# Optimization experiments

Hardware: AMD Instinct MI355X
Metric: run time of the kernel (lower is better)

The kernel has to match this reference:

```python
import jax, jax.numpy as jnp
from jax import lax
import numpy as np

SEQ, BATCH, IN, HID = 512, 256, 248, 1024


def setup_inputs() -> dict:
    key = jax.random.key(0)
    ks = jax.random.split(key, 9)
    s_in = 1.0 / np.sqrt(HID)  # pytorch default init scale for RNN/Linear
    x = jax.random.normal(ks[0], (SEQ, BATCH, IN), dtype=jnp.float32)
    W_ih = jax.random.uniform(ks[1], (HID, IN), jnp.float32, -s_in, s_in)
    b_ih = jax.random.uniform(ks[2], (HID,), jnp.float32, -s_in, s_in)
    W_hh = jax.random.uniform(ks[3], (HID, HID), jnp.float32, -s_in, s_in)
    b_hh = jax.random.uniform(ks[4], (HID,), jnp.float32, -s_in, s_in)
    W_out = jax.random.uniform(ks[5], (1, HID), jnp.float32, -s_in, s_in)
    b_out = jax.random.uniform(ks[6], (1,), jnp.float32, -s_in, s_in)
    w_r = jax.random.uniform(ks[7], (1, 1), jnp.float32, -1.0, 1.0)
    b_r = jax.random.uniform(ks[8], (1,), jnp.float32, -1.0, 1.0)
    return {"x": x, "W_ih": W_ih, "b_ih": b_ih, "W_hh": W_hh, "b_hh": b_hh,
            "W_out": W_out, "b_out": b_out, "w_r": w_r, "b_r": b_r}


def reference(x, W_ih, b_ih, W_hh, b_hh, W_out, b_out, w_r, b_r):
    # x: (T, B, IN) time-major, like torch nn.RNN default.
    T, B, _ = x.shape
    H = W_hh.shape[0]
    # Precompute input projection for all timesteps: (T, B, H)
    xproj = jnp.einsum('tbi,hi->tbh', x, W_ih) + b_ih + b_hh

    def rnn_step(h, xp):
        h_new = jnp.tanh(xp + h @ W_hh.T)
        return h_new, h_new

    h0 = jnp.zeros((B, H), dtype=x.dtype)
    _, hs = lax.scan(rnn_step, h0, xproj)  # hs: (T, B, H)

    # Output logits for all timesteps: (T, B, 1)
    z = jnp.einsum('tbh,oh->tbo', hs, W_out) + b_out

    # o_0 = sigmoid(z_0); o_t = sigmoid(z_t + recurr(o_{t-1}))
    o0 = jax.nn.sigmoid(z[0])

    def out_step(o_prev, zt):
        o = jax.nn.sigmoid(zt + o_prev @ w_r.T + b_r)
        return o, o

    _, os = lax.scan(out_step, o0, z[1:])
    o_all = jnp.concatenate([o0[None], os], axis=0)  # (T, B, 1)
    return o_all[:, :, 0].T  # (B, T), matching oFinal
```

## Files before the change

### kernel.cpp

```cpp
#include <hip/hip_runtime.h>

#define T_SEQ 512
#define NB    256
#define NIN   248
#define NH    1024

typedef __attribute__((ext_vector_type(8))) short          short8;
typedef __attribute__((ext_vector_type(4))) float          f32x4;
typedef __attribute__((ext_vector_type(4))) unsigned int   uint4v;
typedef __attribute__((ext_vector_type(4))) float          float4v;
typedef unsigned long long u64;

#define AS_RELAXED __ATOMIC_RELAXED
#define AS_AGENT   __HIP_MEMORY_SCOPE_AGENT

__device__ __forceinline__ unsigned short f2bf(float f){
  unsigned int u = __float_as_uint(f);
  u += 0x7FFFu + ((u >> 16) & 1u);
  return (unsigned short)(u >> 16);
}

__device__ __forceinline__ float tanh_fast(float v){
  float e = __expf(2.0f * v);
  return 1.0f - 2.0f / (e + 1.0f);
}

__launch_bounds__(256, 1)
__global__ void rnn_scan_kernel(const float* __restrict__ x,
                                const float* __restrict__ W_ih,
                                const float* __restrict__ b_ih,
                                const float* __restrict__ W_hh,
                                const float* __restrict__ b_hh,
                                const float* __restrict__ W_out,
                                unsigned short* __restrict__ hbuf,
                                float* __restrict__ z,
                                unsigned int* __restrict__ bar)
{
  __shared__ alignas(16) unsigned short h_frag[2048 * 8];
  __shared__ alignas(16) unsigned short x_frag[512 * 8];
  __shared__ alignas(8)  unsigned short h_out[16 * 64];
  __shared__ float z_hist[T_SEQ * 16];

  const int tid    = threadIdx.x;
  const int wg     = blockIdx.x;
  const int r16    = wg & 15;
  const int bg     = (r16 & 7) * 2 + (r16 >> 3);
  const int jg     = wg >> 4;
  const int b_base = bg * 16;
  const int l      = tid & 63;
  const int wv     = tid >> 6;
  const int n      = l & 15;
  const int quad   = l >> 4;
  const int j      = jg * 64 + wv * 16 + n;

  unsigned short* h0 = hbuf;
  unsigned short* h1 = hbuf + (size_t)NB * NH;
  unsigned int* ctr  = bar + bg * 32;

  short8 whh[32];
  #pragma unroll
  for (int kt = 0; kt < 32; ++kt){
    const float* p = W_hh + (size_t)j * NH + kt * 32 + quad * 8;
    float4v a = *(const float4v*)p;
    float4v b = *(const float4v*)(p + 4);
    short8 v;
    v[0]=(short)f2bf(a[0]); v[1]=(short)f2bf(a[1]); v[2]=(short)f2bf(a[2]); v[3]=(short)f2bf(a[3]);
    v[4]=(short)f2bf(b[0]); v[5]=(short)f2bf(b[1]); v[6]=(short)f2bf(b[2]); v[7]=(short)f2bf(b[3]);
    whh[kt] = v;
  }
  short8 wih[8];
  #pragma unroll
  for (int kt = 0; kt < 8; ++kt){
    short8 v = {0,0,0,0,0,0,0,0};
    if (!(kt == 7 && quad == 3)){
      const float* p = W_ih + (size_t)j * NIN + kt * 32 + quad * 8;
      float4v a = *(const float4v*)p;
      float4v b = *(const float4v*)(p + 4);
      v[0]=(short)f2bf(a[0]); v[1]=(short)f2bf(a[1]); v[2]=(short)f2bf(a[2]); v[3]=(short)f2bf(a[3]);
      v[4]=(short)f2bf(b[0]); v[5]=(short)f2bf(b[1]); v[6]=(short)f2bf(b[2]); v[7]=(short)f2bf(b[3]);
    }
    wih[kt] = v;
  }
  const float bias  = b_ih[j] + b_hh[j];
  const float woutj = W_out[j];

  #pragma unroll
  for (int i = 0; i < 32; ++i) z_hist[tid + i * 256] = 0.f;
  {
    int r = tid >> 4, c = (tid & 15) * 4;
    __hip_atomic_store((u64*)&h0[(size_t)(b_base + r) * NH + jg * 64 + c],
                       0ull, AS_RELAXED, AS_AGENT);
    int tt = jg * 32 + (tid >> 3);
    int bb = (tid & 7) * 2;
    __hip_atomic_store(&z[(size_t)tt * NB + b_base + bb],     0.f, AS_RELAXED, AS_AGENT);
    __hip_atomic_store(&z[(size_t)tt * NB + b_base + bb + 1], 0.f, AS_RELAXED, AS_AGENT);
  }

  const int xslot_kt[2] = { tid >> 6, (tid + 256) >> 6 };
  const int xslot_l2[2] = { tid & 63, tid & 63 };
  float4v xr[2][2];
  bool    xvalid[2];
  #pragma unroll
  for (int i = 0; i < 2; ++i){
    int kt = xslot_kt[i], l2 = xslot_l2[i];
    int b = b_base + (l2 & 15), k = kt * 32 + (l2 >> 4) * 8;
    xvalid[i] = !(kt == 7 && (l2 >> 4) == 3);
    if (xvalid[i]){
      const float* p = x + ((size_t)0 * NB + b) * NIN + k;
      xr[i][0] = *(const float4v*)p;
      xr[i][1] = *(const float4v*)(p + 4);
    }
  }

  unsigned int target = 16;
  __syncthreads();
  if (tid == 0){
    __hip_atomic_fetch_add(ctr, 1u, AS_RELAXED, AS_AGENT);
    while (__hip_atomic_load(ctr, AS_RELAXED, AS_AGENT) < target)
      __builtin_amdgcn_s_sleep(1);
  }
  __syncthreads();

  for (int t = 0; t < T_SEQ; ++t){
    const unsigned short* hp = (t & 1) ? h1 : h0;
    unsigned short*       hn = (t & 1) ? h0 : h1;

    #pragma unroll
    for (int i = 0; i < 8; ++i){
      int slot = tid + i * 256;
      int kt = slot >> 6, l2 = slot & 63;
      int b = b_base + (l2 & 15), k = kt * 32 + (l2 >> 4) * 8;
      const u64* src = (const u64*)(hp + (size_t)b * NH + k);
      u64 w0 = __hip_atomic_load(src,     AS_RELAXED, AS_AGENT);
      u64 w1 = __hip_atomic_load(src + 1, AS_RELAXED, AS_AGENT);
      u64* dst = (u64*)&h_frag[slot * 8];
      dst[0] = w0; dst[1] = w1;
    }
    #pragma unroll
    for (int i = 0; i < 2; ++i){
      int slot = tid + i * 256;
      uint4v v = {0u,0u,0u,0u};
      if (xvalid[i]){
        v[0] = (unsigned)f2bf(xr[i][0][0]) | ((unsigned)f2bf(xr[i][0][1]) << 16);
        v[1] = (unsigned)f2bf(xr[i][0][2]) | ((unsigned)f2bf(xr[i][0][3]) << 16);
        v[2] = (unsigned)f2bf(xr[i][1][0]) | ((unsigned)f2bf(xr[i][1][1]) << 16);
        v[3] = (unsigned)f2bf(xr[i][1][2]) | ((unsigned)f2bf(xr[i][1][3]) << 16);
      }
      *(uint4v*)&x_frag[slot * 8] = v;
    }
    __syncthreads();

    f32x4 acc0 = {bias, bias, bias, bias};
    f32x4 acc1 = {0.f, 0.f, 0.f, 0.f};
    #pragma unroll
    for (int kt = 0; kt < 32; kt += 2){
      short8 a0 = *(const short8*)&h_frag[(kt * 64 + l) * 8];
      short8 a1 = *(const short8*)&h_frag[((kt + 1) * 64 + l) * 8];
      acc0 = __builtin_amdgcn_mfma_f32_16x16x32_bf16(a0, whh[kt],     acc0, 0, 0, 0);
      acc1 = __builtin_amdgcn_mfma_f32_16x16x32_bf16(a1, whh[kt + 1], acc1, 0, 0, 0);
    }
    #pragma unroll
    for (int kt = 0; kt < 8; kt += 2){
      short8 a0 = *(const short8*)&x_frag[(kt * 64 + l) * 8];
      short8 a1 = *(const short8*)&x_frag[((kt + 1) * 64 + l) * 8];
      acc0 = __builtin_amdgcn_mfma_f32_16x16x32_bf16(a0, wih[kt],     acc0, 0, 0, 0);
      acc1 = __builtin_amdgcn_mfma_f32_16x16x32_bf16(a1, wih[kt + 1], acc1, 0, 0, 0);
    }

    {
      int tn = (t + 1 < T_SEQ) ? t + 1 : t;
      #pragma unroll
      for (int i = 0; i < 2; ++i){
        if (xvalid[i]){
          int kt = xslot_kt[i], l2 = xslot_l2[i];
          int b = b_base + (l2 & 15), k = kt * 32 + (l2 >> 4) * 8;
          const float* p = x + ((size_t)tn * NB + b) * NIN + k;
          xr[i][0] = *(const float4v*)p;
          xr[i][1] = *(const float4v*)(p + 4);
        }
      }
    }

    float hv[4];
    #pragma unroll
    for (int i = 0; i < 4; ++i){
      hv[i] = tanh_fast(acc0[i] + acc1[i]);
      h_out[(quad * 4 + i) * 64 + wv * 16 + n] = f2bf(hv[i]);
    }
    float sv[4];
    #pragma unroll
    for (int i = 0; i < 4; ++i) sv[i] = hv[i] * woutj;
    #pragma unroll
    for (int m = 1; m < 16; m <<= 1){
      #pragma unroll
      for (int i = 0; i < 4; ++i) sv[i] += __shfl_xor(sv[i], m, 64);
    }
    if (n == 0){
      #pragma unroll
      for (int i = 0; i < 4; ++i) atomicAdd(&z_hist[t * 16 + quad * 4 + i], sv[i]);
    }
    __syncthreads();

    {
      int r = tid >> 4, c = (tid & 15) * 4;
      u64 v = *(const u64*)&h_out[r * 64 + c];
      __hip_atomic_store((u64*)&hn[(size_t)(b_base + r) * NH + jg * 64 + c],
                         v, AS_RELAXED, AS_AGENT);
    }

    target += 16;
    __syncthreads();
    if (tid == 0){
      __hip_atomic_fetch_add(ctr, 1u, AS_RELAXED, AS_AGENT);
      while (__hip_atomic_load(ctr, AS_RELAXED, AS_AGENT) < target)
        __builtin_amdgcn_s_sleep(1);
    }
    __syncthreads();
  }

  __syncthreads();
  #pragma unroll
  for (int i = 0; i < 32; ++i){
    int idx = tid + i * 256;
    int tt = idx >> 4, bb = idx & 15;
    atomicAdd(&z[(size_t)tt * NB + b_base + bb], z_hist[idx]);
  }
}

__global__ void out_scan_kernel(const float* __restrict__ z,
                                const float* __restrict__ b_out,
                                const float* __restrict__ w_r,
                                const float* __restrict__ b_r,
                                float* __restrict__ out)
{
  int b = threadIdx.x;
  float bo = b_out[0], wr = w_r[0], br = b_r[0];
  float o = 0.f;
  for (int t = 0; t < T_SEQ; ++t){
    float pre = z[(size_t)t * NB + b] + bo;
    if (t > 0) pre += wr * o + br;
    o = 1.0f / (1.0f + __expf(-pre));
    out[(size_t)b * T_SEQ + t] = o;
  }
}

extern "C" void kernel_launch(void* const* d_in, const int* in_sizes, int n_in,
                              void* d_out, int out_size, void* d_ws, size_t ws_size,
                              hipStream_t stream)
{
  (void)in_sizes; (void)n_in; (void)out_size; (void)ws_size;
  const float* x     = (const float*)d_in[0];
  const float* W_ih  = (const float*)d_in[1];
  const float* b_ih  = (const float*)d_in[2];
  const float* W_hh  = (const float*)d_in[3];
  const float* b_hh  = (const float*)d_in[4];
  const float* W_out = (const float*)d_in[5];
  const float* b_out = (const float*)d_in[6];
  const float* w_r   = (const float*)d_in[7];
  const float* b_r   = (const float*)d_in[8];
  float* out = (float*)d_out;

  unsigned short* hbuf = (unsigned short*)d_ws;
  float* z = (float*)((char*)d_ws + 2 * (size_t)NB * NH * sizeof(unsigned short));
  unsigned int* bar = (unsigned int*)((char*)d_ws
                        + 2 * (size_t)NB * NH * sizeof(unsigned short)
                        + (size_t)T_SEQ * NB * sizeof(float));

  hipMemsetAsync(bar, 0, 16 * 32 * sizeof(unsigned int), stream);

  rnn_scan_kernel<<<dim3(256), dim3(256), 0, stream>>>(
      x, W_ih, b_ih, W_hh, b_hh, W_out, hbuf, z, bar);

  out_scan_kernel<<<dim3(1), dim3(256), 0, stream>>>(z, b_out, w_r, b_r, out);
}
```

Baseline: 2.699 ms.

## Replace counter barrier with per-workgroup step flags and split MFMA accumulators

Replaces the shared fetch-add counter barrier across the 16 workgroups of a batch group with per-workgroup monotonic flags. Each workgroup publishes its step with a store, and every wave polls the 16 flags before loading h, so the atomic RMW contention and the extra block-wide syncs go away. It also batches the global h loads into registers before writing LDS, splits the MFMA chain into four accumulators for more ILP, and moves the W_out reduction after the h store so it overlaps with publication. In exchange it relies on relaxed-ordering visibility of the h stores before the flag store with no explicit fence, and it raises register pressure.

```diff
diff --git a/kernel.cpp b/kernel.cpp
--- a/kernel.cpp
+++ b/kernel.cpp
@@ -55,7 +55,7 @@
 
   unsigned short* h0 = hbuf;
   unsigned short* h1 = hbuf + (size_t)NB * NH;
-  unsigned int* ctr  = bar + bg * 32;
+  unsigned int* flags = bar + bg * 32;
 
   short8 whh[32];
   #pragma unroll
@@ -112,29 +112,30 @@
     }
   }
 
-  unsigned int target = 16;
   __syncthreads();
-  if (tid == 0){
-    __hip_atomic_fetch_add(ctr, 1u, AS_RELAXED, AS_AGENT);
-    while (__hip_atomic_load(ctr, AS_RELAXED, AS_AGENT) < target)
-      __builtin_amdgcn_s_sleep(1);
-  }
-  __syncthreads();
+  if (tid == 0)
+    __hip_atomic_store(&flags[jg], 1u, AS_RELAXED, AS_AGENT);
 
   for (int t = 0; t < T_SEQ; ++t){
     const unsigned short* hp = (t & 1) ? h1 : h0;
     unsigned short*       hn = (t & 1) ? h0 : h1;
 
+    {
+      const unsigned int tgt = (unsigned)(t + 1);
+      const unsigned int* f = &flags[l & 15];
+      while (__hip_atomic_load(f, AS_RELAXED, AS_AGENT) < tgt)
+        __builtin_amdgcn_s_sleep(1);
+    }
+
+    u64 hw0[8], hw1[8];
     #pragma unroll
     for (int i = 0; i < 8; ++i){
       int slot = tid + i * 256;
       int kt = slot >> 6, l2 = slot & 63;
       int b = b_base + (l2 & 15), k = kt * 32 + (l2 >> 4) * 8;
       const u64* src = (const u64*)(hp + (size_t)b * NH + k);
-      u64 w0 = __hip_atomic_load(src,     AS_RELAXED, AS_AGENT);
-      u64 w1 = __hip_atomic_load(src + 1, AS_RELAXED, AS_AGENT);
-      u64* dst = (u64*)&h_frag[slot * 8];
-      dst[0] = w0; dst[1] = w1;
+      hw0[i] = __hip_atomic_load(src,     AS_RELAXED, AS_AGENT);
+      hw1[i] = __hip_atomic_load(src + 1, AS_RELAXED, AS_AGENT);
     }
     #pragma unroll
     for (int i = 0; i < 2; ++i){
@@ -148,23 +149,38 @@
       }
       *(uint4v*)&x_frag[slot * 8] = v;
     }
+    #pragma unroll
+    for (int i = 0; i < 8; ++i){
+      u64* dst = (u64*)&h_frag[(tid + i * 256) * 8];
+      dst[0] = hw0[i]; dst[1] = hw1[i];
+    }
     __syncthreads();
 
-    f32x4 acc0 = {bias, bias, bias, bias};
-    f32x4 acc1 = {0.f, 0.f, 0.f, 0.f};
-    #pragma unroll
-    for (int kt = 0; kt < 32; kt += 2){
-      short8 a0 = *(const short8*)&h_frag[(kt * 64 + l) * 8];
-      short8 a1 = *(const short8*)&h_frag[((kt + 1) * 64 + l) * 8];
-      acc0 = __builtin_amdgcn_mfma_f32_16x16x32_bf16(a0, whh[kt],     acc0, 0, 0, 0);
-      acc1 = __builtin_amdgcn_mfma_f32_16x16x32_bf16(a1, whh[kt + 1], acc1, 0, 0, 0);
-    }
-    #pragma unroll
-    for (int kt = 0; kt < 8; kt += 2){
-      short8 a0 = *(const short8*)&x_frag[(kt * 64 + l) * 8];
-      short8 a1 = *(const short8*)&x_frag[((kt + 1) * 64 + l) * 8];
-      acc0 = __builtin_amdgcn_mfma_f32_16x16x32_bf16(a0, wih[kt],     acc0, 0, 0, 0);
-      acc1 = __builtin_amdgcn_mfma_f32_16x16x32_bf16(a1, wih[kt + 1], acc1, 0, 0, 0);
+    f32x4 a0 = {bias, bias, bias, bias};
+    f32x4 a1 = {0.f, 0.f, 0.f, 0.f};
+    f32x4 a2 = {0.f, 0.f, 0.f, 0.f};
+    f32x4 a3 = {0.f, 0.f, 0.f, 0.f};
+    #pragma unroll
+    for (int kt = 0; kt < 32; kt += 4){
+      short8 f0 = *(const short8*)&h_frag[((kt + 0) * 64 + l) * 8];
+      short8 f1 = *(const short8*)&h_frag[((kt + 1) * 64 + l) * 8];
+      short8 f2 = *(const short8*)&h_frag[((kt + 2) * 64 + l) * 8];
+      short8 f3 = *(const short8*)&h_frag[((kt + 3) * 64 + l) * 8];
+      a0 = __builtin_amdgcn_mfma_f32_16x16x32_bf16(f0, whh[kt + 0], a0, 0, 0, 0);
+      a1 = __builtin_amdgcn_mfma_f32_16x16x32_bf16(f1, whh[kt + 1], a1, 0, 0, 0);
+      a2 = __builtin_amdgcn_mfma_f32_16x16x32_bf16(f2, whh[kt + 2], a2, 0, 0, 0);
+      a3 = __builtin_amdgcn_mfma_f32_16x16x32_bf16(f3, whh[kt + 3], a3, 0, 0, 0);
+    }
+    #pragma unroll
+    for (int kt = 0; kt < 8; kt += 4){
+      short8 f0 = *(const short8*)&x_frag[((kt + 0) * 64 + l) * 8];
+      short8 f1 = *(const short8*)&x_frag[((kt + 1) * 64 + l) * 8];
+      short8 f2 = *(const short8*)&x_frag[((kt + 2) * 64 + l) * 8];
+      short8 f3 = *(const short8*)&x_frag[((kt + 3) * 64 + l) * 8];
+      a0 = __builtin_amdgcn_mfma_f32_16x16x32_bf16(f0, wih[kt + 0], a0, 0, 0, 0);
+      a1 = __builtin_amdgcn_mfma_f32_16x16x32_bf16(f1, wih[kt + 1], a1, 0, 0, 0);
+      a2 = __builtin_amdgcn_mfma_f32_16x16x32_bf16(f2, wih[kt + 2], a2, 0, 0, 0);
+      a3 = __builtin_amdgcn_mfma_f32_16x16x32_bf16(f3, wih[kt + 3], a3, 0, 0, 0);
     }
 
     {
@@ -184,20 +200,8 @@
     float hv[4];
     #pragma unroll
     for (int i = 0; i < 4; ++i){
-      hv[i] = tanh_fast(acc0[i] + acc1[i]);
+      hv[i] = tanh_fast(a0[i] + a1[i] + a2[i] + a3[i]);
       h_out[(quad * 4 + i) * 64 + wv * 16 + n] = f2bf(hv[i]);
-    }
-    float sv[4];
-    #pragma unroll
-    for (int i = 0; i < 4; ++i) sv[i] = hv[i] * woutj;
-    #pragma unroll
-    for (int m = 1; m < 16; m <<= 1){
-      #pragma unroll
-      for (int i = 0; i < 4; ++i) sv[i] += __shfl_xor(sv[i], m, 64);
-    }
-    if (n == 0){
-      #pragma unroll
-      for (int i = 0; i < 4; ++i) atomicAdd(&z_hist[t * 16 + quad * 4 + i], sv[i]);
     }
     __syncthreads();
 
@@ -207,15 +211,22 @@
       __hip_atomic_store((u64*)&hn[(size_t)(b_base + r) * NH + jg * 64 + c],
                          v, AS_RELAXED, AS_AGENT);
     }
-
-    target += 16;
+    float sv[4];
+    #pragma unroll
+    for (int i = 0; i < 4; ++i) sv[i] = hv[i] * woutj;
+    #pragma unroll
+    for (int m = 1; m < 16; m <<= 1){
+      #pragma unroll
+      for (int i = 0; i < 4; ++i) sv[i] += __shfl_xor(sv[i], m, 64);
+    }
+    if (n == 0){
+      #pragma unroll
+      for (int i = 0; i < 4; ++i) atomicAdd(&z_hist[t * 16 + quad * 4 + i], sv[i]);
+    }
+
     __syncthreads();
-    if (tid == 0){
-      __hip_atomic_fetch_add(ctr, 1u, AS_RELAXED, AS_AGENT);
-      while (__hip_atomic_load(ctr, AS_RELAXED, AS_AGENT) < target)
-        __builtin_amdgcn_s_sleep(1);
-    }
-    __syncthreads();
+    if (tid == 0)
+      __hip_atomic_store(&flags[jg], (unsigned)(t + 2), AS_RELAXED, AS_AGENT);
   }
 
   __syncthreads();
```

After: 2.250 ms. 1.2x faster.

## Ping-pong two batch groups per workgroup with per-wave flag barriers

Applied to the files above, without the earlier changes.

Each workgroup now handles two 16-row batch groups (A and B) and alternates between them, so the global h load for one group overlaps the MFMA and tanh work of the other. This hides the latency of the cross-workgroup synchronization. The single counter barrier with s_sleep is replaced by per-wave monotonic flags that every lane polls, which also removes the trailing __syncthreads. The grid is halved to 128 workgroups, which doubles LDS and register use per workgroup. Ordering now rests on relaxed atomics plus vmcnt waits, which carries a memory-ordering risk.

```diff
diff --git a/kernel.cpp b/kernel.cpp
--- a/kernel.cpp
+++ b/kernel.cpp
@@ -19,10 +19,28 @@
   u += 0x7FFFu + ((u >> 16) & 1u);
   return (unsigned short)(u >> 16);
 }
-
+__device__ __forceinline__ unsigned pk2(float lo, float hi){
+  return (unsigned)f2bf(lo) | ((unsigned)f2bf(hi) << 16);
+}
 __device__ __forceinline__ float tanh_fast(float v){
   float e = __expf(2.0f * v);
   return 1.0f - 2.0f / (e + 1.0f);
+}
+
+__device__ __forceinline__ void barrier_lds(){
+  asm volatile("s_waitcnt lgkmcnt(0)" ::: "memory");
+  __builtin_amdgcn_s_barrier();
+  __builtin_amdgcn_sched_barrier(0);
+}
+
+__device__ __forceinline__ void wait_flags(unsigned spec, const unsigned* fl,
+                                           int l, unsigned tgt){
+  if (__all((int)(spec >= tgt))) return;
+  unsigned v;
+  do {
+    __builtin_amdgcn_s_sleep(1);
+    v = __hip_atomic_load(&fl[l], AS_RELAXED, AS_AGENT);
+  } while (!__all((int)(v >= tgt)));
 }
 
 __launch_bounds__(256, 1)
@@ -36,17 +54,20 @@
                                 float* __restrict__ z,
                                 unsigned int* __restrict__ bar)
 {
-  __shared__ alignas(16) unsigned short h_frag[2048 * 8];
-  __shared__ alignas(16) unsigned short x_frag[512 * 8];
-  __shared__ alignas(8)  unsigned short h_out[16 * 64];
-  __shared__ float z_hist[T_SEQ * 16];
+  __shared__ alignas(16) unsigned short h_fragA[2048 * 8];
+  __shared__ alignas(16) unsigned short h_fragB[2048 * 8];
+  __shared__ alignas(16) unsigned short x_fragA[512 * 8];
+  __shared__ alignas(16) unsigned short x_fragB[512 * 8];
+  __shared__ alignas(8)  unsigned short h_out[4 * 256];
+  __shared__ float z_histA[T_SEQ * 16];
+  __shared__ float z_histB[T_SEQ * 16];
 
   const int tid    = threadIdx.x;
   const int wg     = blockIdx.x;
-  const int r16    = wg & 15;
-  const int bg     = (r16 & 7) * 2 + (r16 >> 3);
-  const int jg     = wg >> 4;
-  const int b_base = bg * 16;
+  const int pairId = wg & 7;
+  const int jg     = wg >> 3;
+  const int b_baseA = pairId * 32;
+  const int b_baseB = pairId * 32 + 16;
   const int l      = tid & 63;
   const int wv     = tid >> 6;
   const int n      = l & 15;
@@ -55,7 +76,8 @@
 
   unsigned short* h0 = hbuf;
   unsigned short* h1 = hbuf + (size_t)NB * NH;
-  unsigned int* ctr  = bar + bg * 32;
+  unsigned int* flagsA = bar + pairId * 128;
+  unsigned int* flagsB = bar + pairId * 128 + 64;
 
   short8 whh[32];
   #pragma unroll
@@ -85,137 +107,175 @@
   const float woutj = W_out[j];
 
   #pragma unroll
-  for (int i = 0; i < 32; ++i) z_hist[tid + i * 256] = 0.f;
+  for (int i = 0; i < 32; ++i){
+    z_histA[tid + i * 256] = 0.f;
+    z_histB[tid + i * 256] = 0.f;
+  }
   {
-    int r = tid >> 4, c = (tid & 15) * 4;
-    __hip_atomic_store((u64*)&h0[(size_t)(b_base + r) * NH + jg * 64 + c],
-                       0ull, AS_RELAXED, AS_AGENT);
+    int r = l >> 2, c = (l & 3) * 4;
+    size_t col = (size_t)jg * 64 + wv * 16 + c;
+    __hip_atomic_store((u64*)&h0[(size_t)(b_baseA + r) * NH + col], 0ull, AS_RELAXED, AS_AGENT);
+    __hip_atomic_store((u64*)&h0[(size_t)(b_baseB + r) * NH + col], 0ull, AS_RELAXED, AS_AGENT);
     int tt = jg * 32 + (tid >> 3);
     int bb = (tid & 7) * 2;
-    __hip_atomic_store(&z[(size_t)tt * NB + b_base + bb],     0.f, AS_RELAXED, AS_AGENT);
-    __hip_atomic_store(&z[(size_t)tt * NB + b_base + bb + 1], 0.f, AS_RELAXED, AS_AGENT);
+    __hip_atomic_store(&z[(size_t)tt * NB + b_baseA + bb],     0.f, AS_RELAXED, AS_AGENT);
+    __hip_atomic_store(&z[(size_t)tt * NB + b_baseA + bb + 1], 0.f, AS_RELAXED, AS_AGENT);
+    __hip_atomic_store(&z[(size_t)tt * NB + b_baseB + bb],     0.f, AS_RELAXED, AS_AGENT);
+    __hip_atomic_store(&z[(size_t)tt * NB + b_baseB + bb + 1], 0.f, AS_RELAXED, AS_AGENT);
+  }
+  asm volatile("s_waitcnt vmcnt(0)" ::: "memory");
+  if (l == 0){
+    __hip_atomic_store(&flagsA[jg * 4 + wv], 1u, AS_RELAXED, AS_AGENT);
+    __hip_atomic_store(&flagsB[jg * 4 + wv], 1u, AS_RELAXED, AS_AGENT);
   }
 
   const int xslot_kt[2] = { tid >> 6, (tid + 256) >> 6 };
   const int xslot_l2[2] = { tid & 63, tid & 63 };
-  float4v xr[2][2];
-  bool    xvalid[2];
-  #pragma unroll
-  for (int i = 0; i < 2; ++i){
-    int kt = xslot_kt[i], l2 = xslot_l2[i];
-    int b = b_base + (l2 & 15), k = kt * 32 + (l2 >> 4) * 8;
-    xvalid[i] = !(kt == 7 && (l2 >> 4) == 3);
-    if (xvalid[i]){
-      const float* p = x + ((size_t)0 * NB + b) * NIN + k;
-      xr[i][0] = *(const float4v*)p;
-      xr[i][1] = *(const float4v*)(p + 4);
-    }
-  }
-
-  unsigned int target = 16;
-  __syncthreads();
-  if (tid == 0){
-    __hip_atomic_fetch_add(ctr, 1u, AS_RELAXED, AS_AGENT);
-    while (__hip_atomic_load(ctr, AS_RELAXED, AS_AGENT) < target)
-      __builtin_amdgcn_s_sleep(1);
-  }
-  __syncthreads();
+  bool xvalid[2];
+  #pragma unroll
+  for (int i = 0; i < 2; ++i)
+    xvalid[i] = !(xslot_kt[i] == 7 && (xslot_l2[i] >> 4) == 3);
+
+  float4v xrA[2][2], xrB[2][2];
+  u64 hwA0[8], hwA1[8], hwB0[8], hwB1[8];
+  unsigned fA = 0, fB = 0;
+
+#define XPREF(XR, BBASE, TN)                                               \
+  _Pragma("unroll")                                                        \
+  for (int i = 0; i < 2; ++i){                                             \
+    if (xvalid[i]){                                                        \
+      int kt = xslot_kt[i], l2 = xslot_l2[i];                              \
+      int b = (BBASE) + (l2 & 15), k = kt * 32 + (l2 >> 4) * 8;            \
+      const float* p = x + ((size_t)(TN) * NB + b) * NIN + k;              \
+      XR[i][0] = *(const float4v*)p;                                       \
+      XR[i][1] = *(const float4v*)(p + 4);                                 \
+    }                                                                      \
+  }
+
+#define STAGE_H(HF, HW0, HW1)                                              \
+  _Pragma("unroll")                                                        \
+  for (int i = 0; i < 8; ++i){                                             \
+    u64* dst = (u64*)&HF[(tid + i * 256) * 8];                             \
+    dst[0] = HW0[i]; dst[1] = HW1[i];                                      \
+  }
+
+#define STAGE_X(XF, XR)                                                    \
+  _Pragma("unroll")                                                        \
+  for (int i = 0; i < 2; ++i){                                             \
+    uint4v v = {0u,0u,0u,0u};                                              \
+    if (xvalid[i]){                                                        \
+      v[0] = pk2(XR[i][0][0], XR[i][0][1]);                                \
+      v[1] = pk2(XR[i][0][2], XR[i][0][3]);                                \
+      v[2] = pk2(XR[i][1][0], XR[i][1][1]);                                \
+      v[3] = pk2(XR[i][1][2], XR[i][1][3]);                                \
+    }                                                                      \
+    *(uint4v*)&XF[(tid + i * 256) * 8] = v;                                \
+  }
+
+#define LOAD_H(HW0, HW1, HSRC, BBASE)                                      \
+  _Pragma("unroll")                                                        \
+  for (int i = 0; i < 8; ++i){                                             \
+    int slot = tid + i * 256;                                              \
+    int kt = slot >> 6, l2 = slot & 63;                                    \
+    const u64* src = (const u64*)((HSRC)                                   \
+        + (size_t)((BBASE) + (l2 & 15)) * NH + kt * 32 + (l2 >> 4) * 8);   \
+    HW0[i] = __hip_atomic_load(src,     AS_RELAXED, AS_AGENT);             \
+    HW1[i] = __hip_atomic_load(src + 1, AS_RELAXED, AS_AGENT);             \
+  }
+
+#define MFMA_TILE(HF, XF, A0, A1, A2, A3)                                  \
+  _Pragma("unroll")                                                        \
+  for (int kt = 0; kt < 32; kt += 4){                                      \
+    short8 q0 = *(const short8*)&HF[((kt + 0) * 64 + l) * 8];              \
+    short8 q1 = *(const short8*)&HF[((kt + 1) * 64 + l) * 8];              \
+    short8 q2 = *(const short8*)&HF[((kt + 2) * 64 + l) * 8];              \
+    short8 q3 = *(const short8*)&HF[((kt + 3) * 64 + l) * 8];              \
+    A0 = __builtin_amdgcn_mfma_f32_16x16x32_bf16(q0, whh[kt + 0], A0, 0, 0, 0); \
+    A1 = __builtin_amdgcn_mfma_f32_16x16x32_bf16(q1, whh[kt + 1], A1, 0, 0, 0); \
+    A2 = __builtin_amdgcn_mfma_f32_16x16x32_bf16(q2, whh[kt + 2], A2, 0, 0, 0); \
+    A3 = __builtin_amdgcn_mfma_f32_16x16x32_bf16(q3, whh[kt + 3], A3, 0, 0, 0); \
+  }                                                                        \
+  _Pragma("unroll")                                                        \
+  for (int kt = 0; kt < 8; kt += 4){                                       \
+    short8 q0 = *(const short8*)&XF[((kt + 0) * 64 + l) * 8];              \
+    short8 q1 = *(const short8*)&XF[((kt + 1) * 64 + l) * 8];              \
+    short8 q2 = *(const short8*)&XF[((kt + 2) * 64 + l) * 8];              \
+    short8 q3 = *(const short8*)&XF[((kt + 3) * 64 + l) * 8];              \
+    A0 = __builtin_amdgcn_mfma_f32_16x16x32_bf16(q0, wih[kt + 0], A0, 0, 0, 0); \
+    A1 = __builtin_amdgcn_mfma_f32_16x16x32_bf16(q1, wih[kt + 1], A1, 0, 0, 0); \
+    A2 = __builtin_amdgcn_mfma_f32_16x16x32_bf16(q2, wih[kt + 2], A2, 0, 0, 0); \
+    A3 = __builtin_amdgcn_mfma_f32_16x16x32_bf16(q3, wih[kt + 3], A3, 0, 0, 0); \
+  }
+
+#define FINISH(A0, A1, A2, A3, ZH, BBASE, FLAGS, TPUB)                     \
+  {                                                                        \
+    float sv[4];                                                           \
+    _Pragma("unroll")                                                      \
+    for (int i = 0; i < 4; ++i){                                           \
+      float hvv = tanh_fast(A0[i] + A1[i] + A2[i] + A3[i]);                \
+      h_out[wv * 256 + (quad * 4 + i) * 16 + n] = f2bf(hvv);               \
+      sv[i] = hvv * woutj;                                                 \
+    }                                                                      \
+    _Pragma("unroll")                                                      \
+    for (int m = 1; m < 16; m <<= 1){                                      \
+      _Pragma("unroll")                                                    \
+      for (int i = 0; i < 4; ++i) sv[i] += __shfl_xor(sv[i], m, 64);       \
+    }                                                                      \
+    if (n == 0){                                                           \
+      _Pragma("unroll")                                                    \
+      for (int i = 0; i < 4; ++i)                                          \
+        atomicAdd(&ZH[t * 16 + quad * 4 + i], sv[i]);                      \
+    }                                                                      \
+    {                                                                      \
+      int r = l >> 2, c = (l & 3) * 4;                                     \
+      u64 v = *(const u64*)&h_out[wv * 256 + r * 16 + c];                  \
+      __hip_atomic_store((u64*)&hn[(size_t)((BBASE) + r) * NH              \
+                         + jg * 64 + wv * 16 + c], v, AS_RELAXED, AS_AGENT); \
+    }                                                                      \
+    asm volatile("s_waitcnt vmcnt(0)" ::: "memory");                       \
+    if (l == 0)                                                            \
+      __hip_atomic_store(&FLAGS[jg * 4 + wv], (unsigned)(TPUB),            \
+                         AS_RELAXED, AS_AGENT);                            \
+  }
+
+  wait_flags(0u, flagsA, l, 1u);
+  LOAD_H(hwA0, hwA1, h0, b_baseA);
+  fB = __hip_atomic_load(&flagsB[l], AS_RELAXED, AS_AGENT);
+  XPREF(xrA, b_baseA, 0);
+  XPREF(xrB, b_baseB, 0);
 
   for (int t = 0; t < T_SEQ; ++t){
     const unsigned short* hp = (t & 1) ? h1 : h0;
     unsigned short*       hn = (t & 1) ? h0 : h1;
-
-    #pragma unroll
-    for (int i = 0; i < 8; ++i){
-      int slot = tid + i * 256;
-      int kt = slot >> 6, l2 = slot & 63;
-      int b = b_base + (l2 & 15), k = kt * 32 + (l2 >> 4) * 8;
-      const u64* src = (const u64*)(hp + (size_t)b * NH + k);
-      u64 w0 = __hip_atomic_load(src,     AS_RELAXED, AS_AGENT);
-      u64 w1 = __hip_atomic_load(src + 1, AS_RELAXED, AS_AGENT);
-      u64* dst = (u64*)&h_frag[slot * 8];
-      dst[0] = w0; dst[1] = w1;
-    }
-    #pragma unroll
-    for (int i = 0; i < 2; ++i){
-      int slot = tid + i * 256;
-      uint4v v = {0u,0u,0u,0u};
-      if (xvalid[i]){
-        v[0] = (unsigned)f2bf(xr[i][0][0]) | ((unsigned)f2bf(xr[i][0][1]) << 16);
-        v[1] = (unsigned)f2bf(xr[i][0][2]) | ((unsigned)f2bf(xr[i][0][3]) << 16);
-        v[2] = (unsigned)f2bf(xr[i][1][0]) | ((unsigned)f2bf(xr[i][1][1]) << 16);
-        v[3] = (unsigned)f2bf(xr[i][1][2]) | ((unsigned)f2bf(xr[i][1][3]) << 16);
-      }
-      *(uint4v*)&x_frag[slot * 8] = v;
-    }
-    __syncthreads();
-
-    f32x4 acc0 = {bias, bias, bias, bias};
-    f32x4 acc1 = {0.f, 0.f, 0.f, 0.f};
-    #pragma unroll
-    for (int kt = 0; kt < 32; kt += 2){
-      short8 a0 = *(const short8*)&h_frag[(kt * 64 + l) * 8];
-      short8 a1 = *(const short8*)&h_frag[((kt + 1) * 64 + l) * 8];
-      acc0 = __builtin_amdgcn_mfma_f32_16x16x32_bf16(a0, whh[kt],     acc0, 0, 0, 0);
-      acc1 = __builtin_amdgcn_mfma_f32_16x16x32_bf16(a1, whh[kt + 1], acc1, 0, 0, 0);
-    }
-    #pragma unroll
-    for (int kt = 0; kt < 8; kt += 2){
-      short8 a0 = *(const short8*)&x_frag[(kt * 64 + l) * 8];
-      short8 a1 = *(const short8*)&x_frag[((kt + 1) * 64 + l) * 8];
-      acc0 = __builtin_amdgcn_mfma_f32_16x16x32_bf16(a0, wih[kt],     acc0, 0, 0, 0);
-      acc1 = __builtin_amdgcn_mfma_f32_16x16x32_bf16(a1, wih[kt + 1], acc1, 0, 0, 0);
-    }
-
-    {
-      int tn = (t + 1 < T_SEQ) ? t + 1 : t;
-      #pragma unroll
-      for (int i = 0; i < 2; ++i){
-        if (xvalid[i]){
-          int kt = xslot_kt[i], l2 = xslot_l2[i];
-          int b = b_base + (l2 & 15), k = kt * 32 + (l2 >> 4) * 8;
-          const float* p = x + ((size_t)tn * NB + b) * NIN + k;
-          xr[i][0] = *(const float4v*)p;
-          xr[i][1] = *(const float4v*)(p + 4);
-        }
-      }
-    }
-
-    float hv[4];
-    #pragma unroll
-    for (int i = 0; i < 4; ++i){
-      hv[i] = tanh_fast(acc0[i] + acc1[i]);
-      h_out[(quad * 4 + i) * 64 + wv * 16 + n] = f2bf(hv[i]);
-    }
-    float sv[4];
-    #pragma unroll
-    for (int i = 0; i < 4; ++i) sv[i] = hv[i] * woutj;
-    #pragma unroll
-    for (int m = 1; m < 16; m <<= 1){
-      #pragma unroll
-      for (int i = 0; i < 4; ++i) sv[i] += __shfl_xor(sv[i], m, 64);
-    }
-    if (n == 0){
-      #pragma unroll
-      for (int i = 0; i < 4; ++i) atomicAdd(&z_hist[t * 16 + quad * 4 + i], sv[i]);
-    }
-    __syncthreads();
-
-    {
-      int r = tid >> 4, c = (tid & 15) * 4;
-      u64 v = *(const u64*)&h_out[r * 64 + c];
-      __hip_atomic_store((u64*)&hn[(size_t)(b_base + r) * NH + jg * 64 + c],
-                         v, AS_RELAXED, AS_AGENT);
-    }
-
-    target += 16;
-    __syncthreads();
-    if (tid == 0){
-      __hip_atomic_fetch_add(ctr, 1u, AS_RELAXED, AS_AGENT);
-      while (__hip_atomic_load(ctr, AS_RELAXED, AS_AGENT) < target)
-        __builtin_amdgcn_s_sleep(1);
-    }
-    __syncthreads();
+    const int tn = (t + 1 < T_SEQ) ? t + 1 : t;
+
+    STAGE_H(h_fragA, hwA0, hwA1);
+    wait_flags(fB, flagsB, l, (unsigned)(t + 1));
+    LOAD_H(hwB0, hwB1, hp, b_baseB);
+    STAGE_X(x_fragA, xrA);
+    XPREF(xrA, b_baseA, tn);
+    barrier_lds();
+    f32x4 a0 = {bias, bias, bias, bias};
+    f32x4 a1 = {0.f, 0.f, 0.f, 0.f};
+    f32x4 a2 = {0.f, 0.f, 0.f, 0.f};
+    f32x4 a3 = {0.f, 0.f, 0.f, 0.f};
+    MFMA_TILE(h_fragA, x_fragA, a0, a1, a2, a3);
+    FINISH(a0, a1, a2, a3, z_histA, b_baseA, flagsA, t + 2);
+    fA = __hip_atomic_load(&flagsA[l], AS_RELAXED, AS_AGENT);
+
+    STAGE_H(h_fragB, hwB0, hwB1);
+    wait_flags(fA, flagsA, l, (unsigned)(t + 2));
+    LOAD_H(hwA0, hwA1, hn, b_baseA);
+    STAGE_X(x_fragB, xrB);
+    XPREF(xrB, b_baseB, tn);
+    barrier_lds();
+    f32x4 b0 = {bias, bias, bias, bias};
+    f32x4 b1 = {0.f, 0.f, 0.f, 0.f};
+    f32x4 b2 = {0.f, 0.f, 0.f, 0.f};
+    f32x4 b3 = {0.f, 0.f, 0.f, 0.f};
+    MFMA_TILE(h_fragB, x_fragB, b0, b1, b2, b3);
+    FINISH(b0, b1, b2, b3, z_histB, b_baseB, flagsB, t + 2);
+    fB = __hip_atomic_load(&flagsB[l], AS_RELAXED, AS_AGENT);
   }
 
   __syncthreads();
@@ -223,8 +283,16 @@
   for (int i = 0; i < 32; ++i){
     int idx = tid + i * 256;
     int tt = idx >> 4, bb = idx & 15;
-    atomicAdd(&z[(size_t)tt * NB + b_base + bb], z_hist[idx]);
-  }
+    atomicAdd(&z[(size_t)tt * NB + b_baseA + bb], z_histA[idx]);
+    atomicAdd(&z[(size_t)tt * NB + b_baseB + bb], z_histB[idx]);
+  }
+
+#undef XPREF
+#undef STAGE_H
+#undef STAGE_X
+#undef LOAD_H
+#undef MFMA_TILE
+#undef FINISH
 }
 
 __global__ void out_scan_kernel(const float* __restrict__ z,
@@ -266,9 +334,9 @@
                         + 2 * (size_t)NB * NH * sizeof(unsigned short)
                         + (size_t)T_SEQ * NB * sizeof(float));
 
-  hipMemsetAsync(bar, 0, 16 * 32 * sizeof(unsigned int), stream);
-
-  rnn_scan_kernel<<<dim3(256), dim3(256), 0, stream>>>(
+  hipMemsetAsync(bar, 0, 8 * 128 * sizeof(unsigned int), stream);
+
+  rnn_scan_kernel<<<dim3(128), dim3(256), 0, stream>>>(
       x, W_ih, b_ih, W_hh, b_hh, W_out, hbuf, z, bar);
 
   out_scan_kernel<<<dim3(1), dim3(256), 0, stream>>>(z, b_out, w_r, b_r, out);
```

Measured after the change: 8.654 ms. +220.7%, slower.
